# Kernel optimization log

Measured on AMD Instinct MI355X. Metric: run time of the kernel, lower is better.

Reference implementation:

```python
import jax, jax.numpy as jnp
import numpy as np

EMBED_DIM = 1024
NUM_HEADS = 16
HEAD_DIM = EMBED_DIM // NUM_HEADS


def setup_inputs() -> dict:
    key = jax.random.key(0)
    k_x, k_qw, k_qb, k_ow, k_ob = jax.random.split(key, 5)
    C = EMBED_DIM
    # torch nn.Linear init scale ~ U(-1/sqrt(fan_in), 1/sqrt(fan_in)); use small normals
    s = 1.0 / np.sqrt(C)
    return {
        "x": jax.random.normal(k_x, (4, 2048, C), dtype=jnp.float32),
        "qkv_w": jax.random.uniform(k_qw, (3 * C, C), jnp.float32, -s, s),
        "qkv_b": jax.random.uniform(k_qb, (3 * C,), jnp.float32, -s, s),
        "fc_w": jax.random.uniform(k_ow, (C, C), jnp.float32, -s, s),
        "fc_b": jax.random.uniform(k_ob, (C,), jnp.float32, -s, s),
    }


def reference(x, qkv_w, qkv_b, fc_w, fc_b):
    B, N, C = x.shape
    H, D = NUM_HEADS, HEAD_DIM
    scale = D ** -0.5
    qkv = x @ qkv_w.T + qkv_b                      # [B,N,3C]
    qkv = qkv.reshape(B, N, 3, H, D)
    q, k, v = [jnp.transpose(qkv[:, :, i], (0, 2, 1, 3)) for i in range(3)]  # [B,H,N,D]
    attn = jnp.einsum("bhqd,bhkd->bhqk", q, k) * scale
    attn = jax.nn.softmax(attn, axis=-1)
    out = jnp.einsum("bhqk,bhkd->bhqd", attn, v)   # [B,H,N,D]
    out = jnp.transpose(out, (0, 2, 1, 3)).reshape(B, N, C)
    return out @ fc_w.T + fc_b
```

## Files before the change

### kernel.cpp

```cpp
#include <hip/hip_runtime.h>

#define NUM_HEADS 16
#define HEAD_DIM  64
#define EMB       1024
#define SEQ       2048
#define BATCH     4
#define MROWS     (BATCH * SEQ)
#define QKV_ELEMS (MROWS * EMB)

typedef __attribute__((ext_vector_type(4)))  float  floatx4;
typedef __attribute__((ext_vector_type(16))) float  floatx16;
typedef __attribute__((ext_vector_type(8)))  __bf16 bf16x8;

__device__ __forceinline__ unsigned short f2bf(float f) {
    unsigned int u = __float_as_uint(f);
    u += 0x7fffu + ((u >> 16) & 1u);
    return (unsigned short)(u >> 16);
}

__device__ __forceinline__ ushort4 pk4(float4 v) {
    return make_ushort4(f2bf(v.x), f2bf(v.y), f2bf(v.z), f2bf(v.w));
}

__device__ __forceinline__ uint2 packbf4t(float a0, float a1, float a2, float a3) {
    uint2 r;
    r.x = __builtin_amdgcn_perm(__float_as_uint(a1), __float_as_uint(a0), 0x07060302u);
    r.y = __builtin_amdgcn_perm(__float_as_uint(a3), __float_as_uint(a2), 0x07060302u);
    return r;
}

__device__ __forceinline__ bf16x8 mk8(uint2 lo, uint2 hi) {
    union { uint4 u; bf16x8 b; } cvt;
    cvt.u = make_uint4(lo.x, lo.y, hi.x, hi.y);
    return cvt.b;
}

#define MFMA16(a, b, c) __builtin_amdgcn_mfma_f32_16x16x32_bf16((a), (b), (c), 0, 0, 0)
#define MFMA32(a, b, c) __builtin_amdgcn_mfma_f32_32x32x16_bf16((a), (b), (c), 0, 0, 0)
#define EXP2(x) __builtin_amdgcn_exp2f(x)

__device__ __forceinline__ void async16(const unsigned short* g, unsigned short* l) {
    __builtin_amdgcn_global_load_lds((const __attribute__((address_space(1))) void*)g,
                                     (__attribute__((address_space(3))) void*)l,
                                     16, 0, 0);
}


#define QSCALE 0.18033688011112042f

#define XV4  2097152
#define QWV4 786432
#define FWV4 262144

__global__ __launch_bounds__(256)
void convert_kernel(const float* __restrict__ x, const float* __restrict__ qw,
                    const float* __restrict__ fw,
                    unsigned short* __restrict__ xb, unsigned short* __restrict__ qwb,
                    unsigned short* __restrict__ fwb)
{
    const size_t i = (size_t)blockIdx.x * 256 + threadIdx.x;
    const float* src; unsigned short* dst; size_t off;
    if (i < XV4)              { src = x;  dst = xb;  off = i; }
    else if (i < XV4 + QWV4)  { src = qw; dst = qwb; off = i - XV4; }
    else                      { src = fw; dst = fwb; off = i - (XV4 + QWV4); }
    float4 v = ((const float4*)src)[off];
    ((ushort4*)dst)[off] = pk4(v);
}

__global__ __launch_bounds__(256, 3)
void qkv_kernel(const unsigned short* __restrict__ X, const unsigned short* __restrict__ W,
                const float* __restrict__ BIAS,
                unsigned short* __restrict__ qb, unsigned short* __restrict__ kb,
                unsigned short* __restrict__ vtb)
{
    __shared__ unsigned short As[128 * 32];
    __shared__ unsigned short Bs[128 * 32];

    const int t    = threadIdx.x;
    const int n0   = blockIdx.x * 128;
    const int m0   = blockIdx.y * 128;
    const int wave = t >> 6, lane = t & 63;
    const int wm   = wave & 1, wn = wave >> 1;
    const int l15  = lane & 15, quad = lane >> 4;

    const int srow = wave * 32 + (lane >> 2);
    const int scol = (lane & 3) * 8;
    const int gcol = (((lane & 3) - ((lane >> 3) & 3)) & 3) * 8;
    const unsigned short* gA = X + (size_t)(m0 + srow) * EMB + gcol;
    const unsigned short* gB = W + (size_t)(n0 + srow) * EMB + gcol;
    unsigned short* lA = &As[srow * 32 + scol];
    unsigned short* lB = &Bs[srow * 32 + scol];

    const int arot = (l15 >> 1) & 3;

    const floatx4 zero4 = {0.f, 0.f, 0.f, 0.f};
    floatx4 acc[4][4];
    #pragma unroll
    for (int i = 0; i < 4; ++i)
        #pragma unroll
        for (int j = 0; j < 4; ++j) acc[i][j] = zero4;

    for (int k0 = 0; k0 < EMB; k0 += 32) {
        __syncthreads();
        async16(gA + k0,                     lA);
        async16(gA + k0 + (size_t)16 * EMB,  lA + 16 * 32);
        async16(gB + k0,                     lB);
        async16(gB + k0 + (size_t)16 * EMB,  lB + 16 * 32);
        __syncthreads();

        bf16x8 af[4], bfv[4];
        #pragma unroll
        for (int i = 0; i < 4; ++i) {
            const int pc = ((quad + arot) & 3) * 8;
            af[i]  = *(const bf16x8*)&As[(wm * 64 + i * 16 + l15) * 32 + pc];
            bfv[i] = *(const bf16x8*)&Bs[(wn * 64 + i * 16 + l15) * 32 + pc];
        }
        #pragma unroll
        for (int mi = 0; mi < 4; ++mi)
            #pragma unroll
            for (int ni = 0; ni < 4; ++ni)
                acc[mi][ni] = MFMA16(af[mi], bfv[ni], acc[mi][ni]);
    }

    const int bb = m0 >> 11;
    #pragma unroll
    for (int ni = 0; ni < 4; ++ni) {
        const int gc     = n0 + wn * 64 + ni * 16 + l15;
        const float bias = BIAS[gc];
        const int which  = gc >> 10;
        const int rem    = gc & 1023;
        const int hh     = rem >> 6;
        const int dd     = rem & 63;
        #pragma unroll
        for (int mi = 0; mi < 4; ++mi) {
            const int nseq0 = (m0 & 2047) + wm * 64 + mi * 16 + quad * 4;
            floatx4 v = acc[mi][ni];
            if (which == 2) {
                ushort4 pk;
                pk.x = f2bf(v[0] + bias); pk.y = f2bf(v[1] + bias);
                pk.z = f2bf(v[2] + bias); pk.w = f2bf(v[3] + bias);
                *(ushort4*)&vtb[((size_t)(bb * NUM_HEADS + hh) * HEAD_DIM + dd) * SEQ + nseq0] = pk;
            } else {
                unsigned short* dst = which ? kb : qb;
                const float sc = which ? 1.0f : QSCALE;
                #pragma unroll
                for (int r = 0; r < 4; ++r)
                    dst[((size_t)(bb * NUM_HEADS + hh) * SEQ + (nseq0 + r)) * HEAD_DIM + dd] =
                        f2bf((v[r] + bias) * sc);
            }
        }
    }
}

__global__ __launch_bounds__(256, 4)
void attn_kernel(const unsigned short* __restrict__ qb, const unsigned short* __restrict__ kb,
                 const unsigned short* __restrict__ vtb, unsigned short* __restrict__ attnb)
{
    __shared__ unsigned short smem[16384];

    const int t    = threadIdx.x;
    const int bh   = blockIdx.x;
    const int q0   = blockIdx.y * 128;
    const int b    = bh >> 4, hh = bh & 15;
    const int wave = t >> 6, lane = t & 63;
    const int l31  = lane & 31, hl = lane >> 5;
    const int srow = lane >> 2;
    const int scol = (lane & 3) * 8;
    const int gcol = (((lane & 3) - ((lane >> 3) & 3)) & 3) * 8;
    const int rrot = (l31 >> 1) & 3;

    const unsigned short* qp = qb  + (size_t)bh * SEQ * HEAD_DIM;
    const unsigned short* kp = kb  + (size_t)bh * SEQ * HEAD_DIM;
    const unsigned short* vp = vtb + (size_t)bh * HEAD_DIM * SEQ;

    {
        const int r0 = wave * 32 + srow;
        async16(qp + (size_t)(q0 + r0) * 64 + gcol,           &smem[r0 * 32 + scol]);
        async16(qp + (size_t)(q0 + r0 + 16) * 64 + gcol,      &smem[(r0 + 16) * 32 + scol]);
        async16(qp + (size_t)(q0 + r0) * 64 + 32 + gcol,      &smem[4096 + r0 * 32 + scol]);
        async16(qp + (size_t)(q0 + r0 + 16) * 64 + 32 + gcol, &smem[4096 + (r0 + 16) * 32 + scol]);
    }
    __syncthreads();
    bf16x8 qf[4];
    #pragma unroll
    for (int ks = 0; ks < 4; ++ks)
        qf[ks] = *(const bf16x8*)&smem[(ks >> 1) * 4096 +
                 (wave * 32 + l31) * 32 + ((((ks & 1) * 2 + hl) + rrot) & 3) * 8];

    bf16x8 ones;
    #pragma unroll
    for (int i = 0; i < 8; ++i) ones[i] = (__bf16)1.0f;

    floatx16 o[2], o_sum;
    #pragma unroll
    for (int i = 0; i < 16; ++i) { o[0][i] = 0.f; o[1][i] = 0.f; o_sum[i] = 0.f; }

    for (int kv0 = 0; kv0 < SEQ; kv0 += 128) {
        __syncthreads();
        {
            const int kr = wave * 32 + srow;
            async16(kp + (size_t)(kv0 + kr) * 64 + gcol,           &smem[kr * 32 + scol]);
            async16(kp + (size_t)(kv0 + kr + 16) * 64 + gcol,      &smem[(kr + 16) * 32 + scol]);
            async16(kp + (size_t)(kv0 + kr) * 64 + 32 + gcol,      &smem[4096 + kr * 32 + scol]);
            async16(kp + (size_t)(kv0 + kr + 16) * 64 + 32 + gcol, &smem[4096 + (kr + 16) * 32 + scol]);
            const int vd = wave * 16 + srow;
            #pragma unroll
            for (int kk = 0; kk < 4; ++kk)
                async16(vp + (size_t)vd * SEQ + kv0 + kk * 32 + gcol,
                        &smem[8192 + kk * 2048 + vd * 32 + scol]);
        }
        __syncthreads();

        #pragma unroll
        for (int tt = 0; tt < 4; ++tt) {
            floatx16 st;
            #pragma unroll
            for (int i = 0; i < 16; ++i) st[i] = 0.f;
            #pragma unroll
            for (int ks = 0; ks < 4; ++ks) {
                bf16x8 kf = *(const bf16x8*)&smem[(ks >> 1) * 4096 +
                            (tt * 32 + l31) * 32 + ((((ks & 1) * 2 + hl) + rrot) & 3) * 8];
                st = MFMA32(kf, qf[ks], st);
            }
            uint2 pk0 = packbf4t(EXP2(st[0]),  EXP2(st[1]),  EXP2(st[2]),  EXP2(st[3]));
            uint2 pk1 = packbf4t(EXP2(st[4]),  EXP2(st[5]),  EXP2(st[6]),  EXP2(st[7]));
            uint2 pk2 = packbf4t(EXP2(st[8]),  EXP2(st[9]),  EXP2(st[10]), EXP2(st[11]));
            uint2 pk3 = packbf4t(EXP2(st[12]), EXP2(st[13]), EXP2(st[14]), EXP2(st[15]));

            uint2 xa = hl ? pk0 : pk1;
            xa.x = __shfl_xor(xa.x, 32); xa.y = __shfl_xor(xa.y, 32);
            bf16x8 pfA = hl ? mk8(xa, pk1) : mk8(pk0, xa);
            uint2 xb2 = hl ? pk2 : pk3;
            xb2.x = __shfl_xor(xb2.x, 32); xb2.y = __shfl_xor(xb2.y, 32);
            bf16x8 pfB = hl ? mk8(xb2, pk3) : mk8(pk2, xb2);

            #pragma unroll
            for (int s = 0; s < 2; ++s) {
                const bf16x8 pf = s ? pfB : pfA;
                const int kvblk = tt * 2 + s;
                const int vbase = 8192 + (kvblk >> 1) * 2048;
                const int vchun = ((((kvblk & 1) * 2 + hl) + rrot) & 3) * 8;
                #pragma unroll
                for (int dt = 0; dt < 2; ++dt) {
                    bf16x8 vf = *(const bf16x8*)&smem[vbase + (dt * 32 + l31) * 32 + vchun];
                    o[dt] = MFMA32(pf, vf, o[dt]);
                }
                o_sum = MFMA32(pf, ones, o_sum);
            }
        }
    }

    #pragma unroll
    for (int g = 0; g < 4; ++g)
        #pragma unroll
        for (int e = 0; e < 4; ++e) {
            const float inv  = 1.0f / o_sum[g * 4 + e];
            const int  qrow  = q0 + wave * 32 + e + g * 8 + hl * 4;
            #pragma unroll
            for (int dt = 0; dt < 2; ++dt)
                attnb[(size_t)(b * SEQ + qrow) * EMB + hh * HEAD_DIM + dt * 32 + l31] =
                    f2bf(o[dt][g * 4 + e] * inv);
        }
}

__global__ __launch_bounds__(256, 3)
void proj_kernel(const unsigned short* __restrict__ A, const unsigned short* __restrict__ W,
                 const float* __restrict__ BIAS, float* __restrict__ out)
{
    __shared__ unsigned short As[128 * 32];
    __shared__ unsigned short Bs[128 * 32];

    const int t    = threadIdx.x;
    const int n0   = blockIdx.x * 128;
    const int m0   = blockIdx.y * 128;
    const int wave = t >> 6, lane = t & 63;
    const int wm   = wave & 1, wn = wave >> 1;
    const int l15  = lane & 15, quad = lane >> 4;

    const int srow = wave * 32 + (lane >> 2);
    const int scol = (lane & 3) * 8;
    const int gcol = (((lane & 3) - ((lane >> 3) & 3)) & 3) * 8;
    const unsigned short* gA = A + (size_t)(m0 + srow) * EMB + gcol;
    const unsigned short* gB = W + (size_t)(n0 + srow) * EMB + gcol;
    unsigned short* lA = &As[srow * 32 + scol];
    unsigned short* lB = &Bs[srow * 32 + scol];

    const int arot = (l15 >> 1) & 3;

    const floatx4 zero4 = {0.f, 0.f, 0.f, 0.f};
    floatx4 acc[4][4];
    #pragma unroll
    for (int i = 0; i < 4; ++i)
        #pragma unroll
        for (int j = 0; j < 4; ++j) acc[i][j] = zero4;

    for (int k0 = 0; k0 < EMB; k0 += 32) {
        __syncthreads();
        async16(gA + k0,                     lA);
        async16(gA + k0 + (size_t)16 * EMB,  lA + 16 * 32);
        async16(gB + k0,                     lB);
        async16(gB + k0 + (size_t)16 * EMB,  lB + 16 * 32);
        __syncthreads();

        bf16x8 af[4], bfv[4];
        #pragma unroll
        for (int i = 0; i < 4; ++i) {
            const int pc = ((quad + arot) & 3) * 8;
            af[i]  = *(const bf16x8*)&As[(wm * 64 + i * 16 + l15) * 32 + pc];
            bfv[i] = *(const bf16x8*)&Bs[(wn * 64 + i * 16 + l15) * 32 + pc];
        }
        #pragma unroll
        for (int mi = 0; mi < 4; ++mi)
            #pragma unroll
            for (int ni = 0; ni < 4; ++ni)
                acc[mi][ni] = MFMA16(af[mi], bfv[ni], acc[mi][ni]);
    }

    #pragma unroll
    for (int ni = 0; ni < 4; ++ni) {
        const int gc     = n0 + wn * 64 + ni * 16 + l15;
        const float bias = BIAS[gc];
        #pragma unroll
        for (int mi = 0; mi < 4; ++mi) {
            const int gm = m0 + wm * 64 + mi * 16 + quad * 4;
            #pragma unroll
            for (int r = 0; r < 4; ++r)
                out[(size_t)(gm + r) * EMB + gc] = acc[mi][ni][r] + bias;
        }
    }
}

extern "C" void kernel_launch(void* const* d_in, const int* in_sizes, int n_in,
                              void* d_out, int out_size, void* d_ws, size_t ws_size,
                              hipStream_t stream) {
    (void)in_sizes; (void)n_in; (void)out_size; (void)ws_size;
    const float* x     = (const float*)d_in[0];
    const float* qkv_w = (const float*)d_in[1];
    const float* qkv_b = (const float*)d_in[2];
    const float* fc_w  = (const float*)d_in[3];
    const float* fc_b  = (const float*)d_in[4];
    float* out = (float*)d_out;

    unsigned short* xb    = (unsigned short*)d_ws;
    unsigned short* attnb = xb;
    unsigned short* qbuf  = xb    + QKV_ELEMS;
    unsigned short* kbuf  = qbuf  + QKV_ELEMS;
    unsigned short* vtbuf = kbuf  + QKV_ELEMS;
    unsigned short* qwb   = vtbuf + QKV_ELEMS;
    unsigned short* fwb   = qwb   + 3 * EMB * EMB;

    convert_kernel<<<dim3((XV4 + QWV4 + FWV4) / 256), 256, 0, stream>>>(
        x, qkv_w, fc_w, xb, qwb, fwb);
    qkv_kernel<<<dim3(24, 64), 256, 0, stream>>>(xb, qwb, qkv_b, qbuf, kbuf, vtbuf);
    attn_kernel<<<dim3(64, 16), 256, 0, stream>>>(qbuf, kbuf, vtbuf, attnb);
    proj_kernel<<<dim3(8, 64), 256, 0, stream>>>(attnb, fwb, fc_b, out);
}
```

Measured before the change: 272.7 us.

## Double-buffer K/V tiles in attention and use permlane32 swap

Attention now keeps two shared-memory K/V buffers and prefetches the next 128-row tile asynchronously while computing on the current one, which removes one barrier per iteration and lets the global loads overlap the MFMA work. The shfl_xor exchange between half-waves is replaced with permlane32_swap, and s_setprio raises wave priority around the MFMA sections. Shared memory per block doubles and launch bounds drop from 4 to 2 blocks per CU, which reduces occupancy.

```diff
diff --git a/kernel.cpp b/kernel.cpp
--- a/kernel.cpp
+++ b/kernel.cpp
@@ -152,11 +152,11 @@
     }
 }
 
-__global__ __launch_bounds__(256, 4)
+__global__ __launch_bounds__(256, 2)
 void attn_kernel(const unsigned short* __restrict__ qb, const unsigned short* __restrict__ kb,
                  const unsigned short* __restrict__ vtb, unsigned short* __restrict__ attnb)
 {
-    __shared__ unsigned short smem[16384];
+    __shared__ unsigned short smem[2][16384];
 
     const int t    = threadIdx.x;
     const int bh   = blockIdx.x;
@@ -173,19 +173,34 @@
     const unsigned short* kp = kb  + (size_t)bh * SEQ * HEAD_DIM;
     const unsigned short* vp = vtb + (size_t)bh * HEAD_DIM * SEQ;
 
+    auto stage_kv = [&](int kv0n, unsigned short* B) {
+        const int kr = wave * 32 + srow;
+        async16(kp + (size_t)(kv0n + kr) * 64 + gcol,           &B[kr * 32 + scol]);
+        async16(kp + (size_t)(kv0n + kr + 16) * 64 + gcol,      &B[(kr + 16) * 32 + scol]);
+        async16(kp + (size_t)(kv0n + kr) * 64 + 32 + gcol,      &B[4096 + kr * 32 + scol]);
+        async16(kp + (size_t)(kv0n + kr + 16) * 64 + 32 + gcol, &B[4096 + (kr + 16) * 32 + scol]);
+        const int vd = wave * 16 + srow;
+        #pragma unroll
+        for (int kk = 0; kk < 4; ++kk)
+            async16(vp + (size_t)vd * SEQ + kv0n + kk * 32 + gcol,
+                    &B[8192 + kk * 2048 + vd * 32 + scol]);
+    };
+
     {
         const int r0 = wave * 32 + srow;
-        async16(qp + (size_t)(q0 + r0) * 64 + gcol,           &smem[r0 * 32 + scol]);
-        async16(qp + (size_t)(q0 + r0 + 16) * 64 + gcol,      &smem[(r0 + 16) * 32 + scol]);
-        async16(qp + (size_t)(q0 + r0) * 64 + 32 + gcol,      &smem[4096 + r0 * 32 + scol]);
-        async16(qp + (size_t)(q0 + r0 + 16) * 64 + 32 + gcol, &smem[4096 + (r0 + 16) * 32 + scol]);
+        async16(qp + (size_t)(q0 + r0) * 64 + gcol,           &smem[1][r0 * 32 + scol]);
+        async16(qp + (size_t)(q0 + r0 + 16) * 64 + gcol,      &smem[1][(r0 + 16) * 32 + scol]);
+        async16(qp + (size_t)(q0 + r0) * 64 + 32 + gcol,      &smem[1][4096 + r0 * 32 + scol]);
+        async16(qp + (size_t)(q0 + r0 + 16) * 64 + 32 + gcol, &smem[1][4096 + (r0 + 16) * 32 + scol]);
+        stage_kv(0, smem[0]);
     }
     __syncthreads();
     bf16x8 qf[4];
     #pragma unroll
     for (int ks = 0; ks < 4; ++ks)
-        qf[ks] = *(const bf16x8*)&smem[(ks >> 1) * 4096 +
+        qf[ks] = *(const bf16x8*)&smem[1][(ks >> 1) * 4096 +
                  (wave * 32 + l31) * 32 + ((((ks & 1) * 2 + hl) + rrot) & 3) * 8];
+    __syncthreads();
 
     bf16x8 ones;
     #pragma unroll
@@ -195,45 +210,38 @@
     #pragma unroll
     for (int i = 0; i < 16; ++i) { o[0][i] = 0.f; o[1][i] = 0.f; o_sum[i] = 0.f; }
 
-    for (int kv0 = 0; kv0 < SEQ; kv0 += 128) {
-        __syncthreads();
-        {
-            const int kr = wave * 32 + srow;
-            async16(kp + (size_t)(kv0 + kr) * 64 + gcol,           &smem[kr * 32 + scol]);
-            async16(kp + (size_t)(kv0 + kr + 16) * 64 + gcol,      &smem[(kr + 16) * 32 + scol]);
-            async16(kp + (size_t)(kv0 + kr) * 64 + 32 + gcol,      &smem[4096 + kr * 32 + scol]);
-            async16(kp + (size_t)(kv0 + kr + 16) * 64 + 32 + gcol, &smem[4096 + (kr + 16) * 32 + scol]);
-            const int vd = wave * 16 + srow;
-            #pragma unroll
-            for (int kk = 0; kk < 4; ++kk)
-                async16(vp + (size_t)vd * SEQ + kv0 + kk * 32 + gcol,
-                        &smem[8192 + kk * 2048 + vd * 32 + scol]);
-        }
-        __syncthreads();
+    int cur = 0;
+    for (int it = 0; it < 16; ++it) {
+        if (it < 15) stage_kv((it + 1) * 128, smem[cur ^ 1]);
+
+        const unsigned short* S = smem[cur];
 
         #pragma unroll
         for (int tt = 0; tt < 4; ++tt) {
             floatx16 st;
             #pragma unroll
             for (int i = 0; i < 16; ++i) st[i] = 0.f;
+            __builtin_amdgcn_s_setprio(1);
             #pragma unroll
             for (int ks = 0; ks < 4; ++ks) {
-                bf16x8 kf = *(const bf16x8*)&smem[(ks >> 1) * 4096 +
+                bf16x8 kf = *(const bf16x8*)&S[(ks >> 1) * 4096 +
                             (tt * 32 + l31) * 32 + ((((ks & 1) * 2 + hl) + rrot) & 3) * 8];
                 st = MFMA32(kf, qf[ks], st);
             }
+            __builtin_amdgcn_s_setprio(0);
             uint2 pk0 = packbf4t(EXP2(st[0]),  EXP2(st[1]),  EXP2(st[2]),  EXP2(st[3]));
             uint2 pk1 = packbf4t(EXP2(st[4]),  EXP2(st[5]),  EXP2(st[6]),  EXP2(st[7]));
             uint2 pk2 = packbf4t(EXP2(st[8]),  EXP2(st[9]),  EXP2(st[10]), EXP2(st[11]));
             uint2 pk3 = packbf4t(EXP2(st[12]), EXP2(st[13]), EXP2(st[14]), EXP2(st[15]));
 
-            uint2 xa = hl ? pk0 : pk1;
-            xa.x = __shfl_xor(xa.x, 32); xa.y = __shfl_xor(xa.y, 32);
-            bf16x8 pfA = hl ? mk8(xa, pk1) : mk8(pk0, xa);
-            uint2 xb2 = hl ? pk2 : pk3;
-            xb2.x = __shfl_xor(xb2.x, 32); xb2.y = __shfl_xor(xb2.y, 32);
-            bf16x8 pfB = hl ? mk8(xb2, pk3) : mk8(pk2, xb2);
-
+            auto sA0 = __builtin_amdgcn_permlane32_swap(pk0.x, pk1.x, false, false);
+            auto sA1 = __builtin_amdgcn_permlane32_swap(pk0.y, pk1.y, false, false);
+            auto sB0 = __builtin_amdgcn_permlane32_swap(pk2.x, pk3.x, false, false);
+            auto sB1 = __builtin_amdgcn_permlane32_swap(pk2.y, pk3.y, false, false);
+            bf16x8 pfA = mk8(make_uint2(sA0[0], sA1[0]), make_uint2(sA0[1], sA1[1]));
+            bf16x8 pfB = mk8(make_uint2(sB0[0], sB1[0]), make_uint2(sB0[1], sB1[1]));
+
+            __builtin_amdgcn_s_setprio(1);
             #pragma unroll
             for (int s = 0; s < 2; ++s) {
                 const bf16x8 pf = s ? pfB : pfA;
@@ -242,12 +250,16 @@
                 const int vchun = ((((kvblk & 1) * 2 + hl) + rrot) & 3) * 8;
                 #pragma unroll
                 for (int dt = 0; dt < 2; ++dt) {
-                    bf16x8 vf = *(const bf16x8*)&smem[vbase + (dt * 32 + l31) * 32 + vchun];
+                    bf16x8 vf = *(const bf16x8*)&S[vbase + (dt * 32 + l31) * 32 + vchun];
                     o[dt] = MFMA32(pf, vf, o[dt]);
                 }
                 o_sum = MFMA32(pf, ones, o_sum);
             }
-        }
+            __builtin_amdgcn_s_setprio(0);
+        }
+
+        __syncthreads();
+        cur ^= 1;
     }
 
     #pragma unroll
```

Result: no change. 271.3 us (-0.5%).

## Widen attention blocks to 8 waves sharing K/V tiles and compute row sums on VALU

Applied to the files above, without the earlier changes.

The attention kernel now runs 512-thread blocks that each cover 256 query rows, so every K/V tile loaded into shared memory serves twice as many queries and global K/V traffic drops. The ones-vector MFMA used for softmax denominators is replaced by a VALU sum of the bf16-truncated exponentials, followed by a cross-half reduction and a broadcast. The lane-half exchange now uses permlane32_swap instead of two shuffles, and s_setprio raises wave priority around the MFMA sections. In exchange the code adds more VALU adds and shuffles, keeps more waves resident under the launch bounds, and the truncation only approximates the rounding applied to the packed P values.

```diff
diff --git a/kernel.cpp b/kernel.cpp
--- a/kernel.cpp
+++ b/kernel.cpp
@@ -33,6 +33,10 @@
     union { uint4 u; bf16x8 b; } cvt;
     cvt.u = make_uint4(lo.x, lo.y, hi.x, hi.y);
     return cvt.b;
+}
+
+__device__ __forceinline__ float truncbf(float f) {
+    return __uint_as_float(__float_as_uint(f) & 0xffff0000u);
 }
 
 #define MFMA16(a, b, c) __builtin_amdgcn_mfma_f32_16x16x32_bf16((a), (b), (c), 0, 0, 0)
@@ -152,7 +156,7 @@
     }
 }
 
-__global__ __launch_bounds__(256, 4)
+__global__ __launch_bounds__(512, 6)
 void attn_kernel(const unsigned short* __restrict__ qb, const unsigned short* __restrict__ kb,
                  const unsigned short* __restrict__ vtb, unsigned short* __restrict__ attnb)
 {
@@ -160,7 +164,7 @@
 
     const int t    = threadIdx.x;
     const int bh   = blockIdx.x;
-    const int q0   = blockIdx.y * 128;
+    const int q0   = blockIdx.y * 256;
     const int b    = bh >> 4, hh = bh & 15;
     const int wave = t >> 6, lane = t & 63;
     const int l31  = lane & 31, hl = lane >> 5;
@@ -174,40 +178,39 @@
     const unsigned short* vp = vtb + (size_t)bh * HEAD_DIM * SEQ;
 
     {
-        const int r0 = wave * 32 + srow;
-        async16(qp + (size_t)(q0 + r0) * 64 + gcol,           &smem[r0 * 32 + scol]);
-        async16(qp + (size_t)(q0 + r0 + 16) * 64 + gcol,      &smem[(r0 + 16) * 32 + scol]);
-        async16(qp + (size_t)(q0 + r0) * 64 + 32 + gcol,      &smem[4096 + r0 * 32 + scol]);
-        async16(qp + (size_t)(q0 + r0 + 16) * 64 + 32 + gcol, &smem[4096 + (r0 + 16) * 32 + scol]);
+        const int qr = wave * 16 + srow;
+        #pragma unroll
+        for (int s = 0; s < 2; ++s)
+            #pragma unroll
+            for (int h = 0; h < 2; ++h)
+                async16(qp + (size_t)(q0 + s * 128 + qr) * 64 + h * 32 + gcol,
+                        &smem[s * 8192 + h * 4096 + qr * 32 + scol]);
     }
     __syncthreads();
     bf16x8 qf[4];
     #pragma unroll
     for (int ks = 0; ks < 4; ++ks)
-        qf[ks] = *(const bf16x8*)&smem[(ks >> 1) * 4096 +
-                 (wave * 32 + l31) * 32 + ((((ks & 1) * 2 + hl) + rrot) & 3) * 8];
-
-    bf16x8 ones;
-    #pragma unroll
-    for (int i = 0; i < 8; ++i) ones[i] = (__bf16)1.0f;
-
-    floatx16 o[2], o_sum;
-    #pragma unroll
-    for (int i = 0; i < 16; ++i) { o[0][i] = 0.f; o[1][i] = 0.f; o_sum[i] = 0.f; }
+        qf[ks] = *(const bf16x8*)&smem[(wave >> 2) * 8192 + (ks >> 1) * 4096 +
+                 ((wave & 3) * 32 + l31) * 32 + ((((ks & 1) * 2 + hl) + rrot) & 3) * 8];
+
+    floatx16 o[2];
+    #pragma unroll
+    for (int i = 0; i < 16; ++i) { o[0][i] = 0.f; o[1][i] = 0.f; }
+    float dsum = 0.f;
 
     for (int kv0 = 0; kv0 < SEQ; kv0 += 128) {
         __syncthreads();
         {
-            const int kr = wave * 32 + srow;
-            async16(kp + (size_t)(kv0 + kr) * 64 + gcol,           &smem[kr * 32 + scol]);
-            async16(kp + (size_t)(kv0 + kr + 16) * 64 + gcol,      &smem[(kr + 16) * 32 + scol]);
-            async16(kp + (size_t)(kv0 + kr) * 64 + 32 + gcol,      &smem[4096 + kr * 32 + scol]);
-            async16(kp + (size_t)(kv0 + kr + 16) * 64 + 32 + gcol, &smem[4096 + (kr + 16) * 32 + scol]);
-            const int vd = wave * 16 + srow;
-            #pragma unroll
-            for (int kk = 0; kk < 4; ++kk)
+            const int kr = wave * 16 + srow;
+            async16(kp + (size_t)(kv0 + kr) * 64 + gcol,      &smem[kr * 32 + scol]);
+            async16(kp + (size_t)(kv0 + kr) * 64 + 32 + gcol, &smem[4096 + kr * 32 + scol]);
+            const int kk = wave >> 1;
+            #pragma unroll
+            for (int j = 0; j < 2; ++j) {
+                const int vd = (wave & 1) * 32 + j * 16 + srow;
                 async16(vp + (size_t)vd * SEQ + kv0 + kk * 32 + gcol,
                         &smem[8192 + kk * 2048 + vd * 32 + scol]);
+            }
         }
         __syncthreads();
 
@@ -216,24 +219,45 @@
             floatx16 st;
             #pragma unroll
             for (int i = 0; i < 16; ++i) st[i] = 0.f;
+            __builtin_amdgcn_s_setprio(1);
             #pragma unroll
             for (int ks = 0; ks < 4; ++ks) {
                 bf16x8 kf = *(const bf16x8*)&smem[(ks >> 1) * 4096 +
                             (tt * 32 + l31) * 32 + ((((ks & 1) * 2 + hl) + rrot) & 3) * 8];
                 st = MFMA32(kf, qf[ks], st);
             }
-            uint2 pk0 = packbf4t(EXP2(st[0]),  EXP2(st[1]),  EXP2(st[2]),  EXP2(st[3]));
-            uint2 pk1 = packbf4t(EXP2(st[4]),  EXP2(st[5]),  EXP2(st[6]),  EXP2(st[7]));
-            uint2 pk2 = packbf4t(EXP2(st[8]),  EXP2(st[9]),  EXP2(st[10]), EXP2(st[11]));
-            uint2 pk3 = packbf4t(EXP2(st[12]), EXP2(st[13]), EXP2(st[14]), EXP2(st[15]));
-
-            uint2 xa = hl ? pk0 : pk1;
-            xa.x = __shfl_xor(xa.x, 32); xa.y = __shfl_xor(xa.y, 32);
-            bf16x8 pfA = hl ? mk8(xa, pk1) : mk8(pk0, xa);
-            uint2 xb2 = hl ? pk2 : pk3;
-            xb2.x = __shfl_xor(xb2.x, 32); xb2.y = __shfl_xor(xb2.y, 32);
-            bf16x8 pfB = hl ? mk8(xb2, pk3) : mk8(pk2, xb2);
-
+            __builtin_amdgcn_s_setprio(0);
+
+            float ev[16];
+            #pragma unroll
+            for (int i = 0; i < 16; ++i) ev[i] = EXP2(st[i]);
+
+            {
+                float t0  = truncbf(ev[0]),  t1  = truncbf(ev[1]);
+                float t2  = truncbf(ev[2]),  t3  = truncbf(ev[3]);
+                float t4  = truncbf(ev[4]),  t5  = truncbf(ev[5]);
+                float t6  = truncbf(ev[6]),  t7  = truncbf(ev[7]);
+                float t8  = truncbf(ev[8]),  t9  = truncbf(ev[9]);
+                float t10 = truncbf(ev[10]), t11 = truncbf(ev[11]);
+                float t12 = truncbf(ev[12]), t13 = truncbf(ev[13]);
+                float t14 = truncbf(ev[14]), t15 = truncbf(ev[15]);
+                dsum += (((t0 + t1) + (t2 + t3)) + ((t4 + t5) + (t6 + t7))) +
+                        (((t8 + t9) + (t10 + t11)) + ((t12 + t13) + (t14 + t15)));
+            }
+
+            uint2 pk0 = packbf4t(ev[0],  ev[1],  ev[2],  ev[3]);
+            uint2 pk1 = packbf4t(ev[4],  ev[5],  ev[6],  ev[7]);
+            uint2 pk2 = packbf4t(ev[8],  ev[9],  ev[10], ev[11]);
+            uint2 pk3 = packbf4t(ev[12], ev[13], ev[14], ev[15]);
+
+            auto sA0 = __builtin_amdgcn_permlane32_swap(pk0.x, pk1.x, false, false);
+            auto sA1 = __builtin_amdgcn_permlane32_swap(pk0.y, pk1.y, false, false);
+            auto sB0 = __builtin_amdgcn_permlane32_swap(pk2.x, pk3.x, false, false);
+            auto sB1 = __builtin_amdgcn_permlane32_swap(pk2.y, pk3.y, false, false);
+            bf16x8 pfA = mk8(make_uint2(sA0[0], sA1[0]), make_uint2(sA0[1], sA1[1]));
+            bf16x8 pfB = mk8(make_uint2(sB0[0], sB1[0]), make_uint2(sB0[1], sB1[1]));
+
+            __builtin_amdgcn_s_setprio(1);
             #pragma unroll
             for (int s = 0; s < 2; ++s) {
                 const bf16x8 pf = s ? pfB : pfA;
@@ -245,17 +269,21 @@
                     bf16x8 vf = *(const bf16x8*)&smem[vbase + (dt * 32 + l31) * 32 + vchun];
                     o[dt] = MFMA32(pf, vf, o[dt]);
                 }
-                o_sum = MFMA32(pf, ones, o_sum);
-            }
-        }
-    }
+            }
+            __builtin_amdgcn_s_setprio(0);
+        }
+    }
+
+    float dtot = dsum + __shfl_xor(dsum, 32);
 
     #pragma unroll
     for (int g = 0; g < 4; ++g)
         #pragma unroll
         for (int e = 0; e < 4; ++e) {
-            const float inv  = 1.0f / o_sum[g * 4 + e];
-            const int  qrow  = q0 + wave * 32 + e + g * 8 + hl * 4;
+            const float da  = __shfl(dtot, g * 8 + e);
+            const float db  = __shfl(dtot, g * 8 + e + 4);
+            const float inv = 1.0f / (hl ? db : da);
+            const int  qrow = q0 + wave * 32 + e + g * 8 + hl * 4;
             #pragma unroll
             for (int dt = 0; dt < 2; ++dt)
                 attnb[(size_t)(b * SEQ + qrow) * EMB + hh * HEAD_DIM + dt * 32 + l31] =
@@ -352,6 +380,6 @@
     convert_kernel<<<dim3((XV4 + QWV4 + FWV4) / 256), 256, 0, stream>>>(
         x, qkv_w, fc_w, xb, qwb, fwb);
     qkv_kernel<<<dim3(24, 64), 256, 0, stream>>>(xb, qwb, qkv_b, qbuf, kbuf, vtbuf);
-    attn_kernel<<<dim3(64, 16), 256, 0, stream>>>(qbuf, kbuf, vtbuf, attnb);
+    attn_kernel<<<dim3(64, 8), 512, 0, stream>>>(qbuf, kbuf, vtbuf, attnb);
     proj_kernel<<<dim3(8, 64), 256, 0, stream>>>(attnb, fwb, fc_b, out);
 }
```

After: 371.0 us. 1.36x slower.
